# Optimization experiments

Hardware: AMD Instinct MI355X
Metric: run time of the kernel (lower is better)

The kernel has to match this reference:

```python
import jax, jax.numpy as jnp
import numpy as np

SEL = 20   # selection_length
NN2 = 10   # org_dim*num_library_fns % SEL
NN3 = 22   # org_dim*num_library_fns // SEL - NN2


def _all_combos(L):
    # all 2^L binary vectors of length L; equals union over popcounts of
    # set(itertools.permutations([1]*c + [0]*(L-c))) in the torch code
    ints = jnp.arange(2 ** L, dtype=jnp.uint32)
    bits = (ints[:, None] >> jnp.arange(L, dtype=jnp.uint32)[None, :]) & jnp.uint32(1)
    return bits.astype(jnp.float32)  # [2^L, L]


def _chunk_step(params, combos, combo_sums, prob, chunk):
    """Replicates Model._compute_selarr_output_grad for one chunk.
    params: (W1 [H,L+1], b1 [H], W2 [1,H], b2 [1]) of net2 or net3.
    combos: [N, L] all binary vectors; combo_sums: [N] int popcounts.
    prob: scalar carry probability; chunk: [L] the actual selection.
    """
    W1, b1, W2, b2 = params
    N = combos.shape[0]
    x_all = jnp.concatenate([jnp.full((N, 1), prob, combos.dtype), combos], axis=1)  # [N, L+1]
    h = jnp.tanh(x_all @ W1.T + b1)          # [N, H]
    out = h @ W2[0] + b2[0]                  # [N]
    choices = jnp.round(jnp.sum(chunk)).astype(jnp.int32)
    mask = (combo_sums == choices).astype(combos.dtype)  # valid combinations only
    output_sum = jnp.sum(mask * jnp.exp(out))
    # grad_sum = sum_j out_j * d out_j / d theta (masked), closed form:
    w = mask * out
    s = (1.0 - h * h) * W2[0]                # [N, H]
    gs_W1 = jnp.einsum('n,nh,nd->hd', w, s, x_all)
    gs_b1 = jnp.einsum('n,nh->h', w, s)
    gs_W2 = jnp.einsum('n,nh->h', w, h)[None, :]
    gs_b2 = jnp.sum(w)[None]
    # the key combination = the actual chunk
    xk = jnp.concatenate([prob[None], chunk])
    hk = jnp.tanh(W1 @ xk + b1)
    outk = W2[0] @ hk + b2[0]
    sk = (1.0 - hk * hk) * W2[0]
    p_out = jnp.exp(outk) / output_sum
    grads = (jnp.outer(sk, xk) - gs_W1 / output_sum,
             sk - gs_b1 / output_sum,
             hk[None, :] - gs_W2 / output_sum,
             jnp.ones((1,), xk.dtype) - gs_b2 / output_sum)
    return p_out, grads


def _run_group(params, chunks, prob0):
    L = chunks.shape[1]
    combos = _all_combos(L)
    combo_sums = jnp.round(jnp.sum(combos, axis=1)).astype(jnp.int32)

    def step(carry, chunk):
        prob, acc = carry
        p, g = _chunk_step(params, combos, combo_sums, prob, chunk)
        acc = tuple(a + gi for a, gi in zip(acc, g))
        return (p, acc), p

    acc0 = tuple(jnp.zeros_like(p) for p in params)
    (prob_f, acc), ps = jax.lax.scan(step, (prob0, acc0), chunks)
    return prob_f, acc, ps


def setup_inputs() -> dict:
    key = jax.random.key(0)
    ks = jax.random.split(key, 10)
    total = NN2 * (SEL + 1) + NN3 * SEL  # 650
    selection_arr = jax.random.bernoulli(ks[0], 0.5, (total,)).astype(jnp.float32)
    p0 = jax.random.uniform(ks[1], (1,), jnp.float32)

    def lin(kw, kb, fan_out, fan_in):
        bound = 1.0 / np.sqrt(fan_in)
        W = jax.random.uniform(kw, (fan_out, fan_in), jnp.float32, -bound, bound)
        b = jax.random.uniform(kb, (fan_out,), jnp.float32, -bound, bound)
        return W, b

    W1_2, b1_2 = lin(ks[2], ks[3], 4, SEL + 2)  # net2: Linear(sel+2, 4)
    W2_2, b2_2 = lin(ks[4], ks[5], 1, 4)
    W1_3, b1_3 = lin(ks[6], ks[7], 4, SEL + 1)  # net3: Linear(sel+1, 4)
    W2_3, b2_3 = lin(ks[8], ks[9], 1, 4)
    return {'probability_lib_selection': p0, 'selection_arr': selection_arr,
            'W1_2': W1_2, 'b1_2': b1_2, 'W2_2': W2_2, 'b2_2': b2_2,
            'W1_3': W1_3, 'b1_3': b1_3, 'W2_3': W2_3, 'b2_3': b2_3}


def reference(probability_lib_selection, selection_arr,
              W1_2, b1_2, W2_2, b2_2, W1_3, b1_3, W2_3, b2_3):
    p0 = probability_lib_selection[0]
    n2 = NN2 * (SEL + 1)
    chunks2 = selection_arr[:n2].reshape(NN2, SEL + 1)
    chunks3 = selection_arr[n2:n2 + NN3 * SEL].reshape(NN3, SEL)
    p_after2, g2, ps2 = _run_group((W1_2, b1_2, W2_2, b2_2), chunks2, p0)
    _, g3, ps3 = _run_group((W1_3, b1_3, W2_3, b2_3), chunks3, p_after2)
    sample_probability_array = jnp.concatenate([p0[None], ps2, ps3])  # [1+NN2+NN3]
    return (sample_probability_array,) + g2 + g3
```

## Files before the change

### kernel.cpp

```cpp
#include <hip/hip_runtime.h>
#include <cstdint>
#include <cmath>

#define DEV __device__ __forceinline__

constexpr int SEL = 20;
constexpr int NSTEP2 = 10, NSTEP3 = 22, NSTEPS = 32;
constexpr int L2 = SEL + 1;
constexpr int L3 = SEL;
constexpr int FBE = 7;
constexpr int FBS2 = L2 - FBE;
constexpr int FBS3 = L3 - FBE;
constexpr int BT = 128;

typedef float v2f __attribute__((ext_vector_type(2)));

constexpr float K2E = 2.8853900817779268f;
constexpr float KE  = 1.4426950408889634f;

struct Binom { unsigned v[22][22]; };
constexpr Binom make_binom() {
  Binom b{};
  for (int n = 0; n < 22; n++) {
    b.v[n][0] = 1;
    for (int k = 1; k < 22; k++)
      b.v[n][k] = (k > n) ? 0u : (k == n ? 1u : b.v[n - 1][k - 1] + b.v[n - 1][k]);
  }
  return b;
}
constexpr Binom BN_H = make_binom();
__device__ constexpr Binom BN = make_binom();

constexpr unsigned ceil64u(unsigned x) { return (x + 63u) & ~63u; }
constexpr int padded_count(int NB) {
  int s = 0;
  for (int k = 0; k <= NB; k++) s += (int)ceil64u(BN_H.v[NB][k]);
  return s;
}
constexpr int NPAT2P = padded_count(FBS2);
constexpr int NPAT3P = padded_count(FBS3);

constexpr int SUMS_STRIDE = 96;
constexpr int OFF_SUMS   = 0;
constexpr int OFF_KEYB   = OFF_SUMS + NSTEPS * SUMS_STRIDE;
constexpr int OFF_CT     = OFF_KEYB + 128;
constexpr int OFF_CB     = OFF_CT + 32;
constexpr int OFF_REP    = OFF_CB + 32;
constexpr int OFF_ZEND   = OFF_REP + 32;
constexpr int OFF_TABS   = OFF_ZEND;
constexpr int OFF_PAT2   = OFF_TABS + 3 * 384 * 4;
constexpr int OFF_PAT3   = OFF_PAT2 + NPAT2P;

DEV float fast_tanh(float x) {
  float e = exp2f(x * K2E);
  return 1.0f - 2.0f * __builtin_amdgcn_rcpf(e + 1.0f);
}
DEV float fast_exp(float x) { return exp2f(x * KE); }
DEV void gatomic(float* p, float v) { unsafeAtomicAdd(p, v); }

DEV unsigned gosper(unsigned cmb) {
  unsigned u = cmb & (~cmb + 1u);
  unsigned v = cmb + u;
  return v | ((cmb ^ v) >> (1 + __ffs(u)));
}

DEV float dppsum64(float x) {
  float f = x;
  f += __int_as_float(__builtin_amdgcn_update_dpp(0, __float_as_int(f), 0x111, 0xf, 0xf, false));
  f += __int_as_float(__builtin_amdgcn_update_dpp(0, __float_as_int(f), 0x112, 0xf, 0xf, false));
  f += __int_as_float(__builtin_amdgcn_update_dpp(0, __float_as_int(f), 0x114, 0xf, 0xf, false));
  f += __int_as_float(__builtin_amdgcn_update_dpp(0, __float_as_int(f), 0x118, 0xf, 0xf, false));
  f += __int_as_float(__builtin_amdgcn_update_dpp(0, __float_as_int(f), 0x142, 0xa, 0xf, false));
  f += __int_as_float(__builtin_amdgcn_update_dpp(0, __float_as_int(f), 0x143, 0xc, 0xf, false));
  return f;
}

__global__ void kz(const float* p0, const float* sel,
                   const float* W1_2, const float* b1_2,
                   const float* W1_3, const float* b1_3, float* ws) {
  int tx = threadIdx.x;
  int b = blockIdx.x;
  if (b == 0) {
    __shared__ int sc[NSTEPS];
    for (int i = tx; i < OFF_ZEND; i += blockDim.x) ws[i] = 0.0f;
    __syncthreads();
    if (tx < NSTEPS) {
      int t = tx;
      int g = (t < NSTEP2) ? 0 : 1;
      int L = g ? L3 : L2;
      const float* sbase = sel + (g ? (NSTEP2 * L2 + (t - NSTEP2) * L3) : t * L2);
      unsigned cb = 0; int c = 0;
      for (int d = 0; d < L; d++)
        if (sbase[d] > 0.5f) { cb |= 1u << d; c++; }
      sc[t] = c;
      ((int*)ws)[OFF_CT + t] = c;
      ((unsigned*)ws)[OFF_CB + t] = cb;
      const float* W1 = g ? W1_3 : W1_2;
      const float* b1 = g ? b1_3 : b1_2;
      for (int h = 0; h < 4; h++) {
        float s = b1[h];
        for (int d = 0; d < L; d++)
          if ((cb >> d) & 1) s += W1[h * (L + 1) + 1 + d];
        ws[OFF_KEYB + t * 4 + h] = s;
      }
    }
    __syncthreads();
    if (tx < NSTEPS) {
      int r = tx;
      int start = (tx == 0) ? 0 : ((tx < NSTEP2) ? 1 : NSTEP2);
      for (int u = start; u < tx; u++)
        if (sc[u] == sc[tx]) { r = u; break; }
      ((int*)ws)[OFF_REP + tx] = r;
    }
  } else if (b <= 3) {
    int set = b - 1;
    int LL = (set < 2) ? L2 : L3;
    const float* W1 = (set < 2) ? W1_2 : W1_3;
    const float* b1 = (set < 2) ? b1_2 : b1_3;
    float pval = (set == 0) ? p0[0] : 0.0f;
    int NS1 = 1 << (LL - 14);
    float4* gt = (float4*)(ws + OFF_TABS) + set * 384;
    for (int i = tx; i < 256 + NS1; i += 256) {
      float4 v;
      float* vp = (float*)&v;
      if (i < 128) {
        int e = i;
        for (int h = 0; h < 4; h++) {
          float s = 0;
          for (int j = 0; j < 7; j++) if ((e >> j) & 1) s += W1[h * (LL + 1) + 1 + j];
          vp[h] = exp2f(K2E * s);
        }
      } else if (i < 256) {
        int e = i - 128;
        for (int h = 0; h < 4; h++) {
          float s = b1[h] + pval * W1[h * (LL + 1)];
          for (int j = 0; j < 7; j++) if ((e >> j) & 1) s += W1[h * (LL + 1) + 1 + 7 + j];
          vp[h] = s;
        }
      } else {
        int e = i - 256;
        for (int h = 0; h < 4; h++) {
          float s = 0;
          for (int j = 0; j < LL - 14; j++) if ((e >> j) & 1) s += W1[h * (LL + 1) + 1 + 14 + j];
          vp[h] = s;
        }
      }
      gt[i] = v;
    }
  } else {
    int r = (b - 4) * 256 + tx;
    if (r >= NPAT2P + NPAT3P) return;
    int NB, rr, off;
    if (r < NPAT2P) { NB = FBS2; rr = r; off = OFF_PAT2; }
    else            { NB = FBS3; rr = r - NPAT2P; off = OFF_PAT3; }
    unsigned pat = 0xFFFFFFFFu;
    unsigned base = 0;
    for (int kk = 0; kk <= NB; kk++) {
      unsigned csz = BN.v[NB][kk];
      unsigned psz = (csz + 63u) & ~63u;
      if ((unsigned)rr < base + psz) {
        unsigned local = (unsigned)rr - base;
        if (local < csz) {
          unsigned p2 = 0; int k2 = kk;
          for (int bb = NB - 1; bb >= 0 && k2 > 0; bb--) {
            unsigned cnt = BN.v[bb][k2];
            if (local >= cnt) { p2 |= 1u << bb; local -= cnt; k2--; }
          }
          pat = p2;
        }
        break;
      }
      base += psz;
    }
    ((unsigned*)ws)[off + rr] = pat;
  }
}

constexpr int KC_B2 = NPAT2P / BT;
constexpr int KC_B3 = NPAT3P / BT;
constexpr int KC_BLOCKS = NSTEP2 * KC_B2 + NSTEP3 * KC_B3;

template<int LL>
DEV void kc_work(int t, int sub, int set,
                 const float* W2, const float* b2,
                 float* ws, float4* tabL, float* sS) {
  constexpr int FS = LL - FBE;
  constexpr int NS1 = 1 << (LL - 14);
  constexpr int NS1M = NS1 - 1;
  int tx = threadIdx.x;
  int c = ((const int*)ws)[OFF_CT + t];
  const unsigned* pats = ((const unsigned*)ws) + (LL == 21 ? OFF_PAT2 : OFF_PAT3);
  int pcF = __popc(pats[sub * BT]);
  int pcL = __popc(pats[sub * BT + 64]);
  if (c < pcF || c - pcL > FBE) return;
  const float4* gt = (const float4*)(ws + OFF_TABS) + set * 384;
  for (int i = tx; i < 256 + NS1; i += BT) tabL[i] = gt[i];
  if (tx < SUMS_STRIDE) sS[tx] = 0.0f;
  __syncthreads();
  const float4* tabEX = tabL;
  const float4* tabS0 = tabL + 128;
  const float4* tabS1 = tabL + 256;

  unsigned pat = pats[sub * BT + tx];
  int ce = c - __popc(pat);
  int ce_s = __builtin_amdgcn_readfirstlane(ce);
  int trip = (ce_s >= 0 && ce_s <= FBE) ? (int)BN.v[FBE][ce_s] : 0;
  if (trip > 0) {
    float valid = (ce == ce_s) ? 1.0f : 0.0f;
    float4 vS0 = tabS0[pat & 127];
    float4 vS1 = tabS1[(pat >> 7) & NS1M];
    float E0 = exp2f(K2E * (vS0.x + vS1.x));
    float E1 = exp2f(K2E * (vS0.y + vS1.y));
    float E2 = exp2f(K2E * (vS0.z + vS1.z));
    float E3 = exp2f(K2E * (vS0.w + vS1.w));
    float w0 = W2[0], w1 = W2[1], w2 = W2[2], w3 = W2[3];
    float W0 = b2[0] + w0 + w1 + w2 + w3;
    float m0 = -2.0f * w0, m1 = -2.0f * w1, m2 = -2.0f * w2, m3 = -2.0f * w3;
    float M0 = 4.0f * w0, M1 = 4.0f * w1, M2 = 4.0f * w2, M3 = 4.0f * w3;

    float aE = 0.0f, aW = 0.0f;
    v2f aQa = {0, 0}, aQb = {0, 0}, ORa = {0, 0}, ORb = {0, 0};
#define G_DECL(k) v2f g##k##a = {0, 0}, g##k##b = {0, 0};
    G_DECL(0) G_DECL(1) G_DECL(2) G_DECL(3) G_DECL(4) G_DECL(5) G_DECL(6)
#undef G_DECL

    unsigned ivs = (1u << ce_s) - 1u;
    float4 tE = tabEX[ivs & 127];
#pragma unroll 1
    for (int k = 0; k < trip; k++) {
      float4 cur = tE;
      unsigned ivc = ivs;
      ivs = gosper(ivs);
      tE = tabEX[ivs & 127];
      float r0 = __builtin_amdgcn_rcpf(fmaf(cur.x, E0, 1.0f));
      float r1 = __builtin_amdgcn_rcpf(fmaf(cur.y, E1, 1.0f));
      float r2 = __builtin_amdgcn_rcpf(fmaf(cur.z, E2, 1.0f));
      float r3 = __builtin_amdgcn_rcpf(fmaf(cur.w, E3, 1.0f));
      float outv = W0;
      outv = fmaf(m0, r0, outv); outv = fmaf(m1, r1, outv);
      outv = fmaf(m2, r2, outv); outv = fmaf(m3, r3, outv);
      float e = exp2f(KE * outv) * valid;
      outv *= valid;
      float u0 = fmaf(-r0, r0, r0), u1 = fmaf(-r1, r1, r1);
      float u2 = fmaf(-r2, r2, r2), u3 = fmaf(-r3, r3, r3);
      float q0 = outv * (M0 * u0), q1 = outv * (M1 * u1);
      float q2 = outv * (M2 * u2), q3 = outv * (M3 * u3);
      v2f qa = {q0, q1}, qb = {q2, q3};
      aE += e; aW += outv;
      aQa += qa; aQb += qb;
      ORa += (v2f){outv * r0, outv * r1};
      ORb += (v2f){outv * r2, outv * r3};
#define G_UPD(k) if (ivc & (1u << k)) { g##k##a += qa; g##k##b += qb; }
      G_UPD(0) G_UPD(1) G_UPD(2) G_UPD(3) G_UPD(4) G_UPD(5) G_UPD(6)
#undef G_UPD
    }
    v2f aWHa = {aW - 2.0f * ORa.x, aW - 2.0f * ORa.y};
    v2f aWHb = {aW - 2.0f * ORb.x, aW - 2.0f * ORb.y};

    int lane = tx & 63;
    float rr;
    rr = dppsum64(aE); if (lane == 63 && rr != 0.0f) atomicAdd(&sS[0], rr);
    rr = dppsum64(aW); if (lane == 63 && rr != 0.0f) atomicAdd(&sS[1], rr);
    rr = dppsum64(aQa.x); if (lane == 63 && rr != 0.0f) atomicAdd(&sS[2], rr);
    rr = dppsum64(aQa.y); if (lane == 63 && rr != 0.0f) atomicAdd(&sS[3], rr);
    rr = dppsum64(aQb.x); if (lane == 63 && rr != 0.0f) atomicAdd(&sS[4], rr);
    rr = dppsum64(aQb.y); if (lane == 63 && rr != 0.0f) atomicAdd(&sS[5], rr);
    rr = dppsum64(aWHa.x); if (lane == 63 && rr != 0.0f) atomicAdd(&sS[6], rr);
    rr = dppsum64(aWHa.y); if (lane == 63 && rr != 0.0f) atomicAdd(&sS[7], rr);
    rr = dppsum64(aWHb.x); if (lane == 63 && rr != 0.0f) atomicAdd(&sS[8], rr);
    rr = dppsum64(aWHb.y); if (lane == 63 && rr != 0.0f) atomicAdd(&sS[9], rr);
#define GF(k) { \
    rr = dppsum64(g##k##a.x); if (lane == 63 && rr != 0.0f) atomicAdd(&sS[10 + 0 * 21 + k], rr); \
    rr = dppsum64(g##k##a.y); if (lane == 63 && rr != 0.0f) atomicAdd(&sS[10 + 1 * 21 + k], rr); \
    rr = dppsum64(g##k##b.x); if (lane == 63 && rr != 0.0f) atomicAdd(&sS[10 + 2 * 21 + k], rr); \
    rr = dppsum64(g##k##b.y); if (lane == 63 && rr != 0.0f) atomicAdd(&sS[10 + 3 * 21 + k], rr); }
    GF(0) GF(1) GF(2) GF(3) GF(4) GF(5) GF(6)
#undef GF
#pragma unroll
    for (int j = 0; j < 14; j++) {
      if (j < FS) {
        float m = (float)((pat >> j) & 1u);
        rr = dppsum64(m * aQa.x); if (lane == 63 && rr != 0.0f) atomicAdd(&sS[10 + 0 * 21 + FBE + j], rr);
        rr = dppsum64(m * aQa.y); if (lane == 63 && rr != 0.0f) atomicAdd(&sS[10 + 1 * 21 + FBE + j], rr);
        rr = dppsum64(m * aQb.x); if (lane == 63 && rr != 0.0f) atomicAdd(&sS[10 + 2 * 21 + FBE + j], rr);
        rr = dppsum64(m * aQb.y); if (lane == 63 && rr != 0.0f) atomicAdd(&sS[10 + 3 * 21 + FBE + j], rr);
      }
    }
  }
  __syncthreads();
  if (tx < SUMS_STRIDE) {
    float v = sS[tx];
    if (v != 0.0f) gatomic(&ws[OFF_SUMS + t * SUMS_STRIDE + tx], v);
  }
}

__global__ __launch_bounds__(BT) void kc(
    const float* W2_2, const float* b2_2,
    const float* W2_3, const float* b2_3,
    float* ws) {
  __shared__ float4 tabL[384];
  __shared__ float sS[SUMS_STRIDE];
  int b = blockIdx.x;
  int t, sub;
  if (b < NSTEP2 * KC_B2) { t = b / KC_B2; sub = b % KC_B2; }
  else { int b3 = b - NSTEP2 * KC_B2; t = NSTEP2 + b3 / KC_B3; sub = b3 % KC_B3; }
  int rep = ((const int*)ws)[OFF_REP + t];
  if (rep != t) return;
  if (t < NSTEP2) {
    int set = (t == 0) ? 0 : 1;
    kc_work<21>(t, sub, set, W2_2, b2_2, ws, tabL, sS);
  } else {
    kc_work<20>(t, sub, 2, W2_3, b2_3, ws, tabL, sS);
  }
}

__global__ __launch_bounds__(256) void kd(const float* p0in,
                   const float* W1_2, const float* b1_2, const float* W2_2, const float* b2_2,
                   const float* W1_3, const float* b1_3, const float* W2_3, const float* b2_3,
                   const float* ws, float* out) {
  __shared__ float sS[NSTEPS * SUMS_STRIDE];
  __shared__ float sKEYB[128], sW1c0[8], sW2[8], sB2[2];
  __shared__ float sk_s[NSTEPS][4], hk_s[NSTEPS][4], pp_s[NSTEPS], s0i_s[NSTEPS];
  __shared__ int sREP[NSTEPS];
  int tx = threadIdx.x;
  for (int i = tx; i < NSTEPS * SUMS_STRIDE; i += 256) sS[i] = ws[OFF_SUMS + i];
  for (int i = tx; i < 128; i += 256) sKEYB[i] = ws[OFF_KEYB + i];
  if (tx < NSTEPS) sREP[tx] = ((const int*)ws)[OFF_REP + tx];
  if (tx < 4) {
    sW1c0[tx]     = W1_2[tx * (L2 + 1)];
    sW1c0[4 + tx] = W1_3[tx * (L3 + 1)];
    sW2[tx]     = W2_2[tx];
    sW2[4 + tx] = W2_3[tx];
  }
  if (tx == 0) { sB2[0] = b2_2[0]; sB2[1] = b2_3[0]; }
  __syncthreads();
  if (tx == 0) {
    float p = p0in[0];
    out[0] = p;
    for (int t = 0; t < NSTEPS; t++) {
      int g = (t < NSTEP2) ? 0 : 1;
      pp_s[t] = p;
      float outk = sB2[g];
      for (int h = 0; h < 4; h++)
        outk += sW2[g * 4 + h] * fast_tanh(sKEYB[t * 4 + h] + p * sW1c0[g * 4 + h]);
      float Se = sS[sREP[t] * SUMS_STRIDE + 0];
      p = fast_exp(outk) / Se;
      out[1 + t] = p;
    }
  }
  __syncthreads();
  if (tx < NSTEPS) {
    int t = tx; int g = (t < NSTEP2) ? 0 : 1;
    float p = pp_s[t];
    s0i_s[t] = 1.0f / sS[sREP[t] * SUMS_STRIDE + 0];
    for (int h = 0; h < 4; h++) {
      float hk = fast_tanh(sKEYB[t * 4 + h] + p * sW1c0[g * 4 + h]);
      hk_s[t][h] = hk;
      sk_s[t][h] = (1.0f - hk * hk) * sW2[g * 4 + h];
    }
  }
  __syncthreads();
  const unsigned* cbp = (const unsigned*)ws;
  for (int o = 33 + tx; o < 223; o += blockDim.x) {
    float val = 0.0f;
    if (o < 130) {
      if (o < 121) {
        int e = o - 33; int h = e / 22, d = e % 22;
        for (int t = 0; t < NSTEP2; t++) {
          int rp = sREP[t];
          float xk = (d == 0) ? pp_s[t] : (float)((cbp[OFF_CB + t] >> (d - 1)) & 1);
          float gs = (d == 0) ? pp_s[t] * sS[rp * SUMS_STRIDE + 2 + h]
                              : sS[rp * SUMS_STRIDE + 10 + h * 21 + (d - 1)];
          val += sk_s[t][h] * xk - gs * s0i_s[t];
        }
      } else if (o < 125) { int h = o - 121;
        for (int t = 0; t < NSTEP2; t++) val += sk_s[t][h] - sS[sREP[t] * SUMS_STRIDE + 2 + h] * s0i_s[t];
      } else if (o < 129) { int h = o - 125;
        for (int t = 0; t < NSTEP2; t++) val += hk_s[t][h] - sS[sREP[t] * SUMS_STRIDE + 6 + h] * s0i_s[t];
      } else {
        for (int t = 0; t < NSTEP2; t++) val += 1.0f - sS[sREP[t] * SUMS_STRIDE + 1] * s0i_s[t];
      }
    } else {
      if (o < 214) {
        int e = o - 130; int h = e / 21, d = e % 21;
        for (int t = NSTEP2; t < NSTEPS; t++) {
          int rp = sREP[t];
          float xk = (d == 0) ? pp_s[t] : (float)((cbp[OFF_CB + t] >> (d - 1)) & 1);
          float gs = (d == 0) ? pp_s[t] * sS[rp * SUMS_STRIDE + 2 + h]
                              : sS[rp * SUMS_STRIDE + 10 + h * 21 + (d - 1)];
          val += sk_s[t][h] * xk - gs * s0i_s[t];
        }
      } else if (o < 218) { int h = o - 214;
        for (int t = NSTEP2; t < NSTEPS; t++) val += sk_s[t][h] - sS[sREP[t] * SUMS_STRIDE + 2 + h] * s0i_s[t];
      } else if (o < 222) { int h = o - 218;
        for (int t = NSTEP2; t < NSTEPS; t++) val += hk_s[t][h] - sS[sREP[t] * SUMS_STRIDE + 6 + h] * s0i_s[t];
      } else {
        for (int t = NSTEP2; t < NSTEPS; t++) val += 1.0f - sS[sREP[t] * SUMS_STRIDE + 1] * s0i_s[t];
      }
    }
    out[o] = val;
  }
}

extern "C" void kernel_launch(void* const* d_in, const int* in_sizes, int n_in,
                              void* d_out, int out_size, void* d_ws, size_t ws_size,
                              hipStream_t stream) {
  const float* p0   = (const float*)d_in[0];
  const float* sel  = (const float*)d_in[1];
  const float* W1_2 = (const float*)d_in[2]; const float* b1_2 = (const float*)d_in[3];
  const float* W2_2 = (const float*)d_in[4]; const float* b2_2 = (const float*)d_in[5];
  const float* W1_3 = (const float*)d_in[6]; const float* b1_3 = (const float*)d_in[7];
  const float* W2_3 = (const float*)d_in[8]; const float* b2_3 = (const float*)d_in[9];
  float* out = (float*)d_out;
  float* ws  = (float*)d_ws;
  hipLaunchKernelGGL(kz, dim3(4 + (NPAT2P + NPAT3P + 255) / 256), dim3(256), 0, stream,
                     p0, sel, W1_2, b1_2, W1_3, b1_3, ws);
  hipLaunchKernelGGL(kc, dim3(KC_BLOCKS), dim3(BT), 0, stream,
                     W2_2, b2_2, W2_3, b2_3, ws);
  hipLaunchKernelGGL(kd, dim3(1), dim3(256), 0, stream, p0,
                     W1_2, b1_2, W2_2, b2_2, W1_3, b1_3, W2_3, b2_3, ws, out);
}
```

Measured before the change: 68.43 us.

## Compute tables and patterns inside kc, pack valid chunks densely per block

Moves the per-set lookup tables and combination pattern unranking out of the setup kernel and into each kc block, which builds them in LDS and unranks its own patterns with an LDS binomial table. Blocks now cover four 64-entry chunks mapped compactly through a constexpr chunk map, and each wave handles two chunks, so blocks whose popcount classes cannot match do less work and padded slots are not launched. The setup kernel shrinks to one block. In exchange every active block recomputes the tables redundantly, and each wave runs two sequential inner loops.

```diff
diff --git a/kernel.cpp b/kernel.cpp
--- a/kernel.cpp
+++ b/kernel.cpp
@@ -31,14 +31,24 @@
 constexpr Binom BN_H = make_binom();
 __device__ constexpr Binom BN = make_binom();
 
-constexpr unsigned ceil64u(unsigned x) { return (x + 63u) & ~63u; }
-constexpr int padded_count(int NB) {
-  int s = 0;
-  for (int k = 0; k <= NB; k++) s += (int)ceil64u(BN_H.v[NB][k]);
-  return s;
-}
-constexpr int NPAT2P = padded_count(FBS2);
-constexpr int NPAT3P = padded_count(FBS3);
+struct ChunkMap { int n; unsigned char cls[264]; unsigned short lbase[264]; };
+template<int NB>
+constexpr ChunkMap make_chunkmap() {
+  ChunkMap m{}; int idx = 0;
+  for (int k = 0; k <= NB; k++) {
+    unsigned C = BN_H.v[NB][k];
+    unsigned nch = (C + 63u) / 64u;
+    for (unsigned i = 0; i < nch; i++) {
+      m.cls[idx] = (unsigned char)k;
+      m.lbase[idx] = (unsigned short)(i * 64);
+      idx++;
+    }
+  }
+  m.n = idx;
+  return m;
+}
+__device__ constexpr ChunkMap CM2 = make_chunkmap<FBS2>();
+__device__ constexpr ChunkMap CM3 = make_chunkmap<FBS3>();
 
 constexpr int SUMS_STRIDE = 96;
 constexpr int OFF_SUMS   = 0;
@@ -47,9 +57,6 @@
 constexpr int OFF_CB     = OFF_CT + 32;
 constexpr int OFF_REP    = OFF_CB + 32;
 constexpr int OFF_ZEND   = OFF_REP + 32;
-constexpr int OFF_TABS   = OFF_ZEND;
-constexpr int OFF_PAT2   = OFF_TABS + 3 * 384 * 4;
-constexpr int OFF_PAT3   = OFF_PAT2 + NPAT2P;
 
 DEV float fast_tanh(float x) {
   float e = exp2f(x * K2E);
@@ -62,6 +69,15 @@
   unsigned u = cmb & (~cmb + 1u);
   unsigned v = cmb + u;
   return v | ((cmb ^ v) >> (1 + __ffs(u)));
+}
+
+DEV unsigned unrank_lds(const unsigned* sBN, int NB, int k, unsigned r) {
+  unsigned cmb = 0; int kk = k;
+  for (int bb = NB - 1; bb >= 0 && kk > 0; bb--) {
+    unsigned cnt = sBN[bb * 22 + kk];
+    if (r >= cnt) { cmb |= 1u << bb; r -= cnt; kk--; }
+  }
+  return cmb;
 }
 
 DEV float dppsum64(float x) {
@@ -75,54 +91,72 @@
   return f;
 }
 
-__global__ void kz(const float* p0, const float* sel,
+__global__ __launch_bounds__(256) void kz(const float* p0, const float* sel,
                    const float* W1_2, const float* b1_2,
                    const float* W1_3, const float* b1_3, float* ws) {
   int tx = threadIdx.x;
-  int b = blockIdx.x;
-  if (b == 0) {
-    __shared__ int sc[NSTEPS];
-    for (int i = tx; i < OFF_ZEND; i += blockDim.x) ws[i] = 0.0f;
-    __syncthreads();
-    if (tx < NSTEPS) {
-      int t = tx;
-      int g = (t < NSTEP2) ? 0 : 1;
-      int L = g ? L3 : L2;
-      const float* sbase = sel + (g ? (NSTEP2 * L2 + (t - NSTEP2) * L3) : t * L2);
-      unsigned cb = 0; int c = 0;
+  __shared__ int sc[NSTEPS];
+  for (int i = tx; i < OFF_ZEND; i += 256) ws[i] = 0.0f;
+  __syncthreads();
+  if (tx < NSTEPS) {
+    int t = tx;
+    int g = (t < NSTEP2) ? 0 : 1;
+    int L = g ? L3 : L2;
+    const float* sbase = sel + (g ? (NSTEP2 * L2 + (t - NSTEP2) * L3) : t * L2);
+    unsigned cb = 0; int c = 0;
+    for (int d = 0; d < L; d++)
+      if (sbase[d] > 0.5f) { cb |= 1u << d; c++; }
+    sc[t] = c;
+    ((int*)ws)[OFF_CT + t] = c;
+    ((unsigned*)ws)[OFF_CB + t] = cb;
+    const float* W1 = g ? W1_3 : W1_2;
+    const float* b1 = g ? b1_3 : b1_2;
+    for (int h = 0; h < 4; h++) {
+      float s = b1[h];
       for (int d = 0; d < L; d++)
-        if (sbase[d] > 0.5f) { cb |= 1u << d; c++; }
-      sc[t] = c;
-      ((int*)ws)[OFF_CT + t] = c;
-      ((unsigned*)ws)[OFF_CB + t] = cb;
-      const float* W1 = g ? W1_3 : W1_2;
-      const float* b1 = g ? b1_3 : b1_2;
-      for (int h = 0; h < 4; h++) {
-        float s = b1[h];
-        for (int d = 0; d < L; d++)
-          if ((cb >> d) & 1) s += W1[h * (L + 1) + 1 + d];
-        ws[OFF_KEYB + t * 4 + h] = s;
-      }
-    }
-    __syncthreads();
-    if (tx < NSTEPS) {
-      int r = tx;
-      int start = (tx == 0) ? 0 : ((tx < NSTEP2) ? 1 : NSTEP2);
-      for (int u = start; u < tx; u++)
-        if (sc[u] == sc[tx]) { r = u; break; }
-      ((int*)ws)[OFF_REP + tx] = r;
-    }
-  } else if (b <= 3) {
-    int set = b - 1;
-    int LL = (set < 2) ? L2 : L3;
-    const float* W1 = (set < 2) ? W1_2 : W1_3;
-    const float* b1 = (set < 2) ? b1_2 : b1_3;
-    float pval = (set == 0) ? p0[0] : 0.0f;
-    int NS1 = 1 << (LL - 14);
-    float4* gt = (float4*)(ws + OFF_TABS) + set * 384;
-    for (int i = tx; i < 256 + NS1; i += 256) {
-      float4 v;
-      float* vp = (float*)&v;
+        if ((cb >> d) & 1) s += W1[h * (L + 1) + 1 + d];
+      ws[OFF_KEYB + t * 4 + h] = s;
+    }
+  }
+  __syncthreads();
+  if (tx < NSTEPS) {
+    int r = tx;
+    int start = (tx == 0) ? 0 : ((tx < NSTEP2) ? 1 : NSTEP2);
+    for (int u = start; u < tx; u++)
+      if (sc[u] == sc[tx]) { r = u; break; }
+    ((int*)ws)[OFF_REP + tx] = r;
+  }
+}
+
+constexpr int KCB2 = 66;
+constexpr int KCB3 = 35;
+constexpr int KC_BLOCKS = NSTEP2 * KCB2 + NSTEP3 * KCB3;
+
+template<int LL>
+DEV void kc_work(int t, int sub, float pval,
+                 const float* W1, const float* b1, const float* W2, const float* b2,
+                 float* ws, float4* tabL, unsigned* sBN, float* sS) {
+  constexpr int FS = LL - FBE;
+  constexpr int NS1 = 1 << (LL - 14);
+  constexpr int NS1M = NS1 - 1;
+  const ChunkMap& CM = (LL == 21) ? CM2 : CM3;
+  const int CMN = CM.n;
+  int tx = threadIdx.x;
+  int c = ((const int*)ws)[OFF_CT + t];
+  bool any = false;
+  for (int i = 0; i < 4; i++) {
+    int ci = sub * 4 + i;
+    if (ci < CMN) {
+      int ce = c - (int)CM.cls[ci];
+      if (ce >= 0 && ce <= FBE) any = true;
+    }
+  }
+  if (!any) return;
+  {
+    const unsigned* bnf = &BN.v[0][0];
+    for (int i = tx; i < 484; i += BT) sBN[i] = bnf[i];
+    for (int i = tx; i < 256 + NS1; i += BT) {
+      float4 v; float* vp = (float*)&v;
       if (i < 128) {
         int e = i;
         for (int h = 0; h < 4; h++) {
@@ -145,146 +179,121 @@
           vp[h] = s;
         }
       }
-      gt[i] = v;
-    }
-  } else {
-    int r = (b - 4) * 256 + tx;
-    if (r >= NPAT2P + NPAT3P) return;
-    int NB, rr, off;
-    if (r < NPAT2P) { NB = FBS2; rr = r; off = OFF_PAT2; }
-    else            { NB = FBS3; rr = r - NPAT2P; off = OFF_PAT3; }
-    unsigned pat = 0xFFFFFFFFu;
-    unsigned base = 0;
-    for (int kk = 0; kk <= NB; kk++) {
-      unsigned csz = BN.v[NB][kk];
-      unsigned psz = (csz + 63u) & ~63u;
-      if ((unsigned)rr < base + psz) {
-        unsigned local = (unsigned)rr - base;
-        if (local < csz) {
-          unsigned p2 = 0; int k2 = kk;
-          for (int bb = NB - 1; bb >= 0 && k2 > 0; bb--) {
-            unsigned cnt = BN.v[bb][k2];
-            if (local >= cnt) { p2 |= 1u << bb; local -= cnt; k2--; }
-          }
-          pat = p2;
-        }
-        break;
-      }
-      base += psz;
-    }
-    ((unsigned*)ws)[off + rr] = pat;
-  }
-}
-
-constexpr int KC_B2 = NPAT2P / BT;
-constexpr int KC_B3 = NPAT3P / BT;
-constexpr int KC_BLOCKS = NSTEP2 * KC_B2 + NSTEP3 * KC_B3;
-
-template<int LL>
-DEV void kc_work(int t, int sub, int set,
-                 const float* W2, const float* b2,
-                 float* ws, float4* tabL, float* sS) {
-  constexpr int FS = LL - FBE;
-  constexpr int NS1 = 1 << (LL - 14);
-  constexpr int NS1M = NS1 - 1;
-  int tx = threadIdx.x;
-  int c = ((const int*)ws)[OFF_CT + t];
-  const unsigned* pats = ((const unsigned*)ws) + (LL == 21 ? OFF_PAT2 : OFF_PAT3);
-  int pcF = __popc(pats[sub * BT]);
-  int pcL = __popc(pats[sub * BT + 64]);
-  if (c < pcF || c - pcL > FBE) return;
-  const float4* gt = (const float4*)(ws + OFF_TABS) + set * 384;
-  for (int i = tx; i < 256 + NS1; i += BT) tabL[i] = gt[i];
-  if (tx < SUMS_STRIDE) sS[tx] = 0.0f;
+      tabL[i] = v;
+    }
+    if (tx < SUMS_STRIDE) sS[tx] = 0.0f;
+  }
   __syncthreads();
   const float4* tabEX = tabL;
   const float4* tabS0 = tabL + 128;
   const float4* tabS1 = tabL + 256;
-
-  unsigned pat = pats[sub * BT + tx];
-  int ce = c - __popc(pat);
-  int ce_s = __builtin_amdgcn_readfirstlane(ce);
-  int trip = (ce_s >= 0 && ce_s <= FBE) ? (int)BN.v[FBE][ce_s] : 0;
-  if (trip > 0) {
-    float valid = (ce == ce_s) ? 1.0f : 0.0f;
-    float4 vS0 = tabS0[pat & 127];
-    float4 vS1 = tabS1[(pat >> 7) & NS1M];
-    float E0 = exp2f(K2E * (vS0.x + vS1.x));
-    float E1 = exp2f(K2E * (vS0.y + vS1.y));
-    float E2 = exp2f(K2E * (vS0.z + vS1.z));
-    float E3 = exp2f(K2E * (vS0.w + vS1.w));
-    float w0 = W2[0], w1 = W2[1], w2 = W2[2], w3 = W2[3];
-    float W0 = b2[0] + w0 + w1 + w2 + w3;
-    float m0 = -2.0f * w0, m1 = -2.0f * w1, m2 = -2.0f * w2, m3 = -2.0f * w3;
-    float M0 = 4.0f * w0, M1 = 4.0f * w1, M2 = 4.0f * w2, M3 = 4.0f * w3;
-
-    float aE = 0.0f, aW = 0.0f;
-    v2f aQa = {0, 0}, aQb = {0, 0}, ORa = {0, 0}, ORb = {0, 0};
+  int lane = tx & 63, wid = tx >> 6;
+
+  float w0 = W2[0], w1 = W2[1], w2 = W2[2], w3 = W2[3];
+  float W0 = b2[0] + w0 + w1 + w2 + w3;
+  float m0 = -2.0f * w0, m1 = -2.0f * w1, m2 = -2.0f * w2, m3 = -2.0f * w3;
+  float M0 = 4.0f * w0, M1 = 4.0f * w1, M2 = 4.0f * w2, M3 = 4.0f * w3;
+
+  float aE = 0.0f, aW = 0.0f;
+  v2f ORa = {0, 0}, ORb = {0, 0};
 #define G_DECL(k) v2f g##k##a = {0, 0}, g##k##b = {0, 0};
-    G_DECL(0) G_DECL(1) G_DECL(2) G_DECL(3) G_DECL(4) G_DECL(5) G_DECL(6)
+  G_DECL(0) G_DECL(1) G_DECL(2) G_DECL(3) G_DECL(4) G_DECL(5) G_DECL(6)
 #undef G_DECL
 
-    unsigned ivs = (1u << ce_s) - 1u;
-    float4 tE = tabEX[ivs & 127];
-#pragma unroll 1
-    for (int k = 0; k < trip; k++) {
-      float4 cur = tE;
-      unsigned ivc = ivs;
-      ivs = gosper(ivs);
-      tE = tabEX[ivs & 127];
-      float r0 = __builtin_amdgcn_rcpf(fmaf(cur.x, E0, 1.0f));
-      float r1 = __builtin_amdgcn_rcpf(fmaf(cur.y, E1, 1.0f));
-      float r2 = __builtin_amdgcn_rcpf(fmaf(cur.z, E2, 1.0f));
-      float r3 = __builtin_amdgcn_rcpf(fmaf(cur.w, E3, 1.0f));
-      float outv = W0;
-      outv = fmaf(m0, r0, outv); outv = fmaf(m1, r1, outv);
-      outv = fmaf(m2, r2, outv); outv = fmaf(m3, r3, outv);
-      float e = exp2f(KE * outv) * valid;
-      outv *= valid;
-      float u0 = fmaf(-r0, r0, r0), u1 = fmaf(-r1, r1, r1);
-      float u2 = fmaf(-r2, r2, r2), u3 = fmaf(-r3, r3, r3);
-      float q0 = outv * (M0 * u0), q1 = outv * (M1 * u1);
-      float q2 = outv * (M2 * u2), q3 = outv * (M3 * u3);
-      v2f qa = {q0, q1}, qb = {q2, q3};
-      aE += e; aW += outv;
-      aQa += qa; aQb += qb;
-      ORa += (v2f){outv * r0, outv * r1};
-      ORb += (v2f){outv * r2, outv * r3};
-#define G_UPD(k) if (ivc & (1u << k)) { g##k##a += qa; g##k##b += qb; }
-      G_UPD(0) G_UPD(1) G_UPD(2) G_UPD(3) G_UPD(4) G_UPD(5) G_UPD(6)
-#undef G_UPD
-    }
-    v2f aWHa = {aW - 2.0f * ORa.x, aW - 2.0f * ORa.y};
-    v2f aWHb = {aW - 2.0f * ORb.x, aW - 2.0f * ORb.y};
-
-    int lane = tx & 63;
-    float rr;
-    rr = dppsum64(aE); if (lane == 63 && rr != 0.0f) atomicAdd(&sS[0], rr);
-    rr = dppsum64(aW); if (lane == 63 && rr != 0.0f) atomicAdd(&sS[1], rr);
-    rr = dppsum64(aQa.x); if (lane == 63 && rr != 0.0f) atomicAdd(&sS[2], rr);
-    rr = dppsum64(aQa.y); if (lane == 63 && rr != 0.0f) atomicAdd(&sS[3], rr);
-    rr = dppsum64(aQb.x); if (lane == 63 && rr != 0.0f) atomicAdd(&sS[4], rr);
-    rr = dppsum64(aQb.y); if (lane == 63 && rr != 0.0f) atomicAdd(&sS[5], rr);
-    rr = dppsum64(aWHa.x); if (lane == 63 && rr != 0.0f) atomicAdd(&sS[6], rr);
-    rr = dppsum64(aWHa.y); if (lane == 63 && rr != 0.0f) atomicAdd(&sS[7], rr);
-    rr = dppsum64(aWHb.x); if (lane == 63 && rr != 0.0f) atomicAdd(&sS[8], rr);
-    rr = dppsum64(aWHb.y); if (lane == 63 && rr != 0.0f) atomicAdd(&sS[9], rr);
+#define DO_CHUNK(id) \
+  v2f cQa##id = {0, 0}, cQb##id = {0, 0}; unsigned pat##id = 0; \
+  { int ci = sub * 4 + wid * 2 + id; \
+    if (ci < CMN) { \
+      int k = (int)CM.cls[ci]; \
+      int ce = c - k; \
+      if (ce >= 0 && ce <= FBE) { \
+        unsigned Ck = sBN[FS * 22 + k]; \
+        unsigned myr = (unsigned)CM.lbase[ci] + (unsigned)lane; \
+        float valid = (myr < Ck) ? 1.0f : 0.0f; \
+        unsigned pr = (myr < Ck) ? myr : (Ck - 1u); \
+        unsigned pp = unrank_lds(sBN, FS, k, pr); \
+        pat##id = pp; \
+        float4 vS0 = tabS0[pp & 127]; \
+        float4 vS1 = tabS1[(pp >> 7) & NS1M]; \
+        float E0 = exp2f(K2E * (vS0.x + vS1.x)); \
+        float E1 = exp2f(K2E * (vS0.y + vS1.y)); \
+        float E2 = exp2f(K2E * (vS0.z + vS1.z)); \
+        float E3 = exp2f(K2E * (vS0.w + vS1.w)); \
+        int trip = (int)sBN[FBE * 22 + ce]; \
+        unsigned ivs = (1u << ce) - 1u; \
+        float4 tE = tabEX[ivs & 127]; \
+        _Pragma("unroll 1") \
+        for (int kk = 0; kk < trip; kk++) { \
+          float4 cur = tE; \
+          unsigned ivc = ivs; \
+          ivs = gosper(ivs); \
+          tE = tabEX[ivs & 127]; \
+          float r0 = __builtin_amdgcn_rcpf(fmaf(cur.x, E0, 1.0f)); \
+          float r1 = __builtin_amdgcn_rcpf(fmaf(cur.y, E1, 1.0f)); \
+          float r2 = __builtin_amdgcn_rcpf(fmaf(cur.z, E2, 1.0f)); \
+          float r3 = __builtin_amdgcn_rcpf(fmaf(cur.w, E3, 1.0f)); \
+          float outv = W0; \
+          outv = fmaf(m0, r0, outv); outv = fmaf(m1, r1, outv); \
+          outv = fmaf(m2, r2, outv); outv = fmaf(m3, r3, outv); \
+          float e = exp2f(KE * outv) * valid; \
+          outv *= valid; \
+          float u0 = fmaf(-r0, r0, r0), u1 = fmaf(-r1, r1, r1); \
+          float u2 = fmaf(-r2, r2, r2), u3 = fmaf(-r3, r3, r3); \
+          float q0 = outv * (M0 * u0), q1 = outv * (M1 * u1); \
+          float q2 = outv * (M2 * u2), q3 = outv * (M3 * u3); \
+          v2f qa = {q0, q1}, qb = {q2, q3}; \
+          aE += e; aW += outv; \
+          cQa##id += qa; cQb##id += qb; \
+          ORa += (v2f){outv * r0, outv * r1}; \
+          ORb += (v2f){outv * r2, outv * r3}; \
+          if (ivc & 1u)  { g0a += qa; g0b += qb; } \
+          if (ivc & 2u)  { g1a += qa; g1b += qb; } \
+          if (ivc & 4u)  { g2a += qa; g2b += qb; } \
+          if (ivc & 8u)  { g3a += qa; g3b += qb; } \
+          if (ivc & 16u) { g4a += qa; g4b += qb; } \
+          if (ivc & 32u) { g5a += qa; g5b += qb; } \
+          if (ivc & 64u) { g6a += qa; g6b += qb; } \
+        } \
+      } } }
+  DO_CHUNK(0)
+  DO_CHUNK(1)
+#undef DO_CHUNK
+
+  v2f aQa = cQa0 + cQa1, aQb = cQb0 + cQb1;
+  v2f aWHa = {aW - 2.0f * ORa.x, aW - 2.0f * ORa.y};
+  v2f aWHb = {aW - 2.0f * ORb.x, aW - 2.0f * ORb.y};
+
+  float rr;
+  rr = dppsum64(aE); if (lane == 63 && rr != 0.0f) atomicAdd(&sS[0], rr);
+  rr = dppsum64(aW); if (lane == 63 && rr != 0.0f) atomicAdd(&sS[1], rr);
+  rr = dppsum64(aQa.x); if (lane == 63 && rr != 0.0f) atomicAdd(&sS[2], rr);
+  rr = dppsum64(aQa.y); if (lane == 63 && rr != 0.0f) atomicAdd(&sS[3], rr);
+  rr = dppsum64(aQb.x); if (lane == 63 && rr != 0.0f) atomicAdd(&sS[4], rr);
+  rr = dppsum64(aQb.y); if (lane == 63 && rr != 0.0f) atomicAdd(&sS[5], rr);
+  rr = dppsum64(aWHa.x); if (lane == 63 && rr != 0.0f) atomicAdd(&sS[6], rr);
+  rr = dppsum64(aWHa.y); if (lane == 63 && rr != 0.0f) atomicAdd(&sS[7], rr);
+  rr = dppsum64(aWHb.x); if (lane == 63 && rr != 0.0f) atomicAdd(&sS[8], rr);
+  rr = dppsum64(aWHb.y); if (lane == 63 && rr != 0.0f) atomicAdd(&sS[9], rr);
 #define GF(k) { \
-    rr = dppsum64(g##k##a.x); if (lane == 63 && rr != 0.0f) atomicAdd(&sS[10 + 0 * 21 + k], rr); \
-    rr = dppsum64(g##k##a.y); if (lane == 63 && rr != 0.0f) atomicAdd(&sS[10 + 1 * 21 + k], rr); \
-    rr = dppsum64(g##k##b.x); if (lane == 63 && rr != 0.0f) atomicAdd(&sS[10 + 2 * 21 + k], rr); \
-    rr = dppsum64(g##k##b.y); if (lane == 63 && rr != 0.0f) atomicAdd(&sS[10 + 3 * 21 + k], rr); }
-    GF(0) GF(1) GF(2) GF(3) GF(4) GF(5) GF(6)
+  rr = dppsum64(g##k##a.x); if (lane == 63 && rr != 0.0f) atomicAdd(&sS[10 + 0 * 21 + k], rr); \
+  rr = dppsum64(g##k##a.y); if (lane == 63 && rr != 0.0f) atomicAdd(&sS[10 + 1 * 21 + k], rr); \
+  rr = dppsum64(g##k##b.x); if (lane == 63 && rr != 0.0f) atomicAdd(&sS[10 + 2 * 21 + k], rr); \
+  rr = dppsum64(g##k##b.y); if (lane == 63 && rr != 0.0f) atomicAdd(&sS[10 + 3 * 21 + k], rr); }
+  GF(0) GF(1) GF(2) GF(3) GF(4) GF(5) GF(6)
 #undef GF
 #pragma unroll
-    for (int j = 0; j < 14; j++) {
-      if (j < FS) {
-        float m = (float)((pat >> j) & 1u);
-        rr = dppsum64(m * aQa.x); if (lane == 63 && rr != 0.0f) atomicAdd(&sS[10 + 0 * 21 + FBE + j], rr);
-        rr = dppsum64(m * aQa.y); if (lane == 63 && rr != 0.0f) atomicAdd(&sS[10 + 1 * 21 + FBE + j], rr);
-        rr = dppsum64(m * aQb.x); if (lane == 63 && rr != 0.0f) atomicAdd(&sS[10 + 2 * 21 + FBE + j], rr);
-        rr = dppsum64(m * aQb.y); if (lane == 63 && rr != 0.0f) atomicAdd(&sS[10 + 3 * 21 + FBE + j], rr);
-      }
+  for (int j = 0; j < 14; j++) {
+    if (j < FS) {
+      float b0f = (float)((pat0 >> j) & 1u);
+      float b1f = (float)((pat1 >> j) & 1u);
+      float vax = fmaf(b0f, cQa0.x, b1f * cQa1.x);
+      float vay = fmaf(b0f, cQa0.y, b1f * cQa1.y);
+      float vbx = fmaf(b0f, cQb0.x, b1f * cQb1.x);
+      float vby = fmaf(b0f, cQb0.y, b1f * cQb1.y);
+      rr = dppsum64(vax); if (lane == 63 && rr != 0.0f) atomicAdd(&sS[10 + 0 * 21 + FBE + j], rr);
+      rr = dppsum64(vay); if (lane == 63 && rr != 0.0f) atomicAdd(&sS[10 + 1 * 21 + FBE + j], rr);
+      rr = dppsum64(vbx); if (lane == 63 && rr != 0.0f) atomicAdd(&sS[10 + 2 * 21 + FBE + j], rr);
+      rr = dppsum64(vby); if (lane == 63 && rr != 0.0f) atomicAdd(&sS[10 + 3 * 21 + FBE + j], rr);
     }
   }
   __syncthreads();
@@ -295,22 +304,23 @@
 }
 
 __global__ __launch_bounds__(BT) void kc(
-    const float* W2_2, const float* b2_2,
-    const float* W2_3, const float* b2_3,
+    const float* p0,
+    const float* W1_2, const float* b1_2, const float* W2_2, const float* b2_2,
+    const float* W1_3, const float* b1_3, const float* W2_3, const float* b2_3,
     float* ws) {
   __shared__ float4 tabL[384];
+  __shared__ unsigned sBN[484];
   __shared__ float sS[SUMS_STRIDE];
   int b = blockIdx.x;
   int t, sub;
-  if (b < NSTEP2 * KC_B2) { t = b / KC_B2; sub = b % KC_B2; }
-  else { int b3 = b - NSTEP2 * KC_B2; t = NSTEP2 + b3 / KC_B3; sub = b3 % KC_B3; }
-  int rep = ((const int*)ws)[OFF_REP + t];
-  if (rep != t) return;
+  if (b < NSTEP2 * KCB2) { t = b / KCB2; sub = b % KCB2; }
+  else { int b3 = b - NSTEP2 * KCB2; t = NSTEP2 + b3 / KCB3; sub = b3 % KCB3; }
+  if (((const int*)ws)[OFF_REP + t] != t) return;
   if (t < NSTEP2) {
-    int set = (t == 0) ? 0 : 1;
-    kc_work<21>(t, sub, set, W2_2, b2_2, ws, tabL, sS);
+    float pval = (t == 0) ? p0[0] : 0.0f;
+    kc_work<21>(t, sub, pval, W1_2, b1_2, W2_2, b2_2, ws, tabL, sBN, sS);
   } else {
-    kc_work<20>(t, sub, 2, W2_3, b2_3, ws, tabL, sS);
+    kc_work<20>(t, sub, 0.0f, W1_3, b1_3, W2_3, b2_3, ws, tabL, sBN, sS);
   }
 }
 
@@ -413,10 +423,10 @@
   const float* W2_3 = (const float*)d_in[8]; const float* b2_3 = (const float*)d_in[9];
   float* out = (float*)d_out;
   float* ws  = (float*)d_ws;
-  hipLaunchKernelGGL(kz, dim3(4 + (NPAT2P + NPAT3P + 255) / 256), dim3(256), 0, stream,
+  hipLaunchKernelGGL(kz, dim3(1), dim3(256), 0, stream,
                      p0, sel, W1_2, b1_2, W1_3, b1_3, ws);
-  hipLaunchKernelGGL(kc, dim3(KC_BLOCKS), dim3(BT), 0, stream,
-                     W2_2, b2_2, W2_3, b2_3, ws);
+  hipLaunchKernelGGL(kc, dim3(KC_BLOCKS), dim3(BT), 0, stream, p0,
+                     W1_2, b1_2, W2_2, b2_2, W1_3, b1_3, W2_3, b2_3, ws);
   hipLaunchKernelGGL(kd, dim3(1), dim3(256), 0, stream, p0,
                      W1_2, b1_2, W2_2, b2_2, W1_3, b1_3, W2_3, b2_3, ws, out);
 }
```

Result: slower. 80.62 us (+17.8%).
